# Kernel optimization log

Hardware: AMD Instinct MI355X
Metric: run time of the kernel (lower is better)

The kernel has to match this reference:

```python
import jax, jax.numpy as jnp
import numpy as np

# 20 amino-acid letters and per-residue atom counts (len(struct.atoms) - 1 in the source)
LETTERS = "ARNDCQEGHILKMFPSTWYV"
RES_LEN = {"A": 4, "R": 10, "N": 7, "D": 7, "C": 5, "Q": 8, "E": 8, "G": 3, "H": 9,
           "I": 7, "L": 7, "K": 8, "M": 7, "F": 10, "P": 6, "S": 5, "T": 6, "W": 13,
           "Y": 11, "V": 6}
BATCH = 16
N_RES = 1024       # number of residues (output 'nodes')
ATOM_DIM = 64
AMINO_DIM = 256
INDS = 1           # one trailing (3,) tensor axis


def make_metadata():
    """Deterministic protein sequence + per-letter gather indices (static numpy)."""
    rng = np.random.default_rng(42)
    seq = rng.integers(0, len(LETTERS), size=N_RES)
    lens = np.array([RES_LEN[LETTERS[s]] for s in seq])
    starts = np.concatenate([[0], np.cumsum(lens)[:-1]])  # residue_indices
    atoms = int(lens.sum())
    # group residues by letter: (residue positions, atom gather indices (n_l, L))
    groups = {}
    for li, letter in enumerate(LETTERS):
        pos = np.where(seq == li)[0]
        if len(pos) == 0:
            continue
        L = RES_LEN[letter]
        idx = starts[pos][:, None] + np.arange(L)[None, :]  # (n_l, L)
        groups[letter] = (pos, idx)
    # static row offsets of each letter's weight block inside the flat weight
    offsets, off = {}, 0
    for letter in LETTERS:
        offsets[letter] = off
        off += RES_LEN[letter] * ATOM_DIM
    return atoms, groups, offsets


def setup_inputs() -> dict:
    atoms, groups, offsets = make_metadata()
    key = jax.random.key(0)
    k1, k2 = jax.random.split(key)
    x = jax.random.normal(k1, (BATCH, atoms, ATOM_DIM, 3), dtype=jnp.float32)
    total_rows = sum(RES_LEN[l] for l in LETTERS) * ATOM_DIM  # 147*64 = 9408
    W = jax.random.normal(k2, (total_rows, AMINO_DIM), dtype=jnp.float32)
    # per-expert 1/sqrt(fan_in) init scaling
    scale = np.zeros((total_rows, 1), np.float32)
    for l in LETTERS:
        fan = RES_LEN[l] * ATOM_DIM
        scale[offsets[l]:offsets[l] + fan] = 1.0 / np.sqrt(fan)
    W = W * jnp.asarray(scale)
    return {"x": x, "W_flat": W}


def reference(x, W_flat):
    """x: (B, atoms, D, 3); W_flat: (sum_l L_l*D, amino_dim).
    Equivalent to per-residue slice -> reshape -> per-letter TensLinear -> stack,
    but grouped by letter into batched GEMMs (same math, reordered)."""
    atoms, groups, offsets = make_metadata()
    B = x.shape[0]
    out = jnp.zeros((B, N_RES, AMINO_DIM, 3), dtype=x.dtype)
    for letter, (pos, idx) in groups.items():  # fixed loop over <=20 expert types
        L = RES_LEN[letter]
        fan = L * ATOM_DIM
        g = x[:, idx]                              # (B, n_l, L, D, 3) gather
        g = g.reshape(B, len(pos), fan, 3)         # flatten residue atoms x channels
        Wl = W_flat[offsets[letter]:offsets[letter] + fan]  # (fan, amino_dim)
        y = jnp.einsum("bnki,ko->bnoi", g, Wl)     # (B, n_l, amino_dim, 3)
        out = out.at[:, pos].set(y)                # scatter back into residue order
    return out
```

## Files before the change

### kernel.cpp

```cpp
#include <hip/hip_runtime.h>
#include <hip/hip_bf16.h>
#include <cstdint>
#include <cstddef>

#define NRES 1024
#define NB 16
#define ADIM 64
#define ODIM 256
#define TOTROWS 9408

typedef __bf16 bf16x8 __attribute__((ext_vector_type(8)));
typedef float f32x4 __attribute__((ext_vector_type(4)));

struct Meta {
    uint16_t start[NRES];
    uint8_t  letter[NRES];
    int atoms;
};

constexpr int RES_LEN_A[20] = {4,10,7,7,5,8,8,3,9,7,7,8,7,10,6,5,6,13,11,6};

constexpr uint32_t ss_hash(uint32_t value, uint32_t& hc) {
    value ^= hc;
    hc *= 0x931e8875u;
    value *= hc;
    value ^= value >> 16;
    return value;
}
constexpr uint32_t ss_mix(uint32_t x, uint32_t y) {
    uint32_t r = 0xca01f9ddu * x - 0x4973f715u * y;
    r ^= r >> 16;
    return r;
}

constexpr Meta make_meta() {
    Meta m = {};
    uint32_t pool[4] = {0,0,0,0};
    uint32_t hc = 0x43b0d7e5u;
    pool[0] = ss_hash(42u, hc);
    pool[1] = ss_hash(0u, hc);
    pool[2] = ss_hash(0u, hc);
    pool[3] = ss_hash(0u, hc);
    for (int s = 0; s < 4; ++s)
        for (int d = 0; d < 4; ++d)
            if (s != d) pool[d] = ss_mix(pool[d], ss_hash(pool[s], hc));
    uint32_t hb = 0x8b51f9ddu;
    uint64_t w[8] = {};
    for (int i = 0; i < 8; ++i) {
        uint32_t dv = pool[i & 3] ^ hb;
        hb *= 0x58f38dedu;
        dv *= hb;
        dv ^= dv >> 16;
        w[i] = dv;
    }
    uint64_t s64[4] = {};
    for (int i = 0; i < 4; ++i) s64[i] = w[2*i] | (w[2*i+1] << 32);
    using u128 = unsigned __int128;
    const u128 MULT = ((u128)2549297995355413924ULL << 64) | (u128)4865540595714422341ULL;
    u128 initstate = ((u128)s64[0] << 64) | (u128)s64[1];
    u128 initseq   = ((u128)s64[2] << 64) | (u128)s64[3];
    u128 inc = (initseq << 1) | (u128)1;
    u128 state = inc;
    state += initstate;
    state = state * MULT + inc;
    bool has32 = false;
    uint32_t cached = 0;
    int atoms = 0;
    for (int i = 0; i < NRES; ++i) {
        uint32_t res = 0;
        while (true) {
            uint32_t r32;
            if (has32) { r32 = cached; has32 = false; }
            else {
                state = state * MULT + inc;
                uint64_t hi = (uint64_t)(state >> 64);
                uint64_t lo = (uint64_t)state;
                uint32_t rot = (uint32_t)(state >> 122);
                uint64_t v = hi ^ lo;
                uint64_t o64 = (v >> rot) | (v << ((64u - rot) & 63u));
                cached = (uint32_t)(o64 >> 32);
                has32 = true;
                r32 = (uint32_t)o64;
            }
            uint64_t mm = (uint64_t)r32 * 20ull;
            uint32_t leftover = (uint32_t)mm;
            if (leftover >= 16u) { res = (uint32_t)(mm >> 32); break; }
        }
        m.letter[i] = (uint8_t)res;
        m.start[i] = (uint16_t)atoms;
        atoms += RES_LEN_A[res];
    }
    m.atoms = atoms;
    return m;
}

constexpr Meta H_META = make_meta();

struct LetterTab {
    int woff[21];
    int fan[20];
};
constexpr LetterTab make_tab() {
    LetterTab t = {};
    int off = 0;
    for (int l = 0; l < 20; ++l) {
        t.woff[l] = off;
        t.fan[l] = RES_LEN_A[l] * ADIM;
        off += t.fan[l];
    }
    t.woff[20] = off;
    return t;
}

struct Perm { uint16_t p[NRES]; };
constexpr Perm make_perm() {
    int ord[20];
    for (int i = 0; i < 20; ++i) ord[i] = i;
    for (int a = 0; a < 20; ++a) {
        int best = a;
        for (int j = a + 1; j < 20; ++j)
            if (RES_LEN_A[ord[j]] > RES_LEN_A[ord[best]]) best = j;
        int t = ord[a]; ord[a] = ord[best]; ord[best] = t;
    }
    Perm pr = {};
    int n = 0;
    for (int oi = 0; oi < 20; ++oi) {
        const int l = ord[oi];
        for (int p = 0; p < NRES; ++p)
            if (H_META.letter[p] == l) pr.p[n++] = (uint16_t)p;
    }
    return pr;
}

__constant__ Meta g_meta = make_meta();
__constant__ LetterTab g_tab = make_tab();
__constant__ Perm g_perm = make_perm();

__device__ __bf16 g_Wt[(size_t)TOTROWS * ODIM];

__global__ __launch_bounds__(256) void prep_W_kernel(const float* __restrict__ W) {
    const int tid = threadIdx.x;
    const int b = blockIdx.x * 4 + (tid >> 6);
    const int lane = tid & 63;
    const int l15 = lane & 15;
    const int g4 = lane >> 4;

    int l = 0;
    while (b >= (g_tab.woff[l + 1] >> 1)) ++l;
    const int rel = b - (g_tab.woff[l] >> 1);
    const int c = rel >> 5;
    const int r32 = rel & 31;
    const int h = r32 >> 4;
    const int wv = (r32 >> 2) & 3;
    const int nt = r32 & 3;

    const int n = wv * 64 + nt * 16 + l15;
    const int kg = g_tab.woff[l] + c * 64 + h * 32 + g4 * 8;

    bf16x8 v;
    #pragma unroll
    for (int q = 0; q < 8; ++q)
        v[q] = (__bf16)W[(size_t)(kg + q) * ODIM + n];
    *(bf16x8*)&g_Wt[(size_t)b * 512 + (size_t)(l15 * 4 + g4) * 8] = v;
}

__device__ __forceinline__ void gload16(const void* g, void* l) {
    __builtin_amdgcn_global_load_lds(
        (const __attribute__((address_space(1))) uint32_t*)(uintptr_t)g,
        (__attribute__((address_space(3))) uint32_t*)(uint32_t)(uintptr_t)l,
        16, 0, 0);
}

__global__ __launch_bounds__(512) void lin_mfma_kernel(const float* __restrict__ x,
                                                       float* __restrict__ out,
                                                       int atoms) {
    const int p = g_perm.p[blockIdx.x];
    const int letter = g_meta.letter[p];
    const int start = g_meta.start[p];
    const int fan = g_tab.fan[letter];
    const __bf16* wslab = g_Wt + (size_t)g_tab.woff[letter] * ODIM;

    const int tid = threadIdx.x;
    const int lane = tid & 63;
    const int w8 = tid >> 6;
    const int l15 = lane & 15;
    const int g4 = lane >> 4;

    __shared__ __align__(16) uint8_t raw[2 * 12288];
    __shared__ __align__(16) __bf16 As[2][48][72];

    const float* xb = x + (size_t)start * 192;
    const size_t bstrB = (size_t)atoms * 768;
    const int nc = fan >> 6;

    const int s0 = 2 * w8, s1 = s0 + 1;
    const uint32_t pos0 = (uint32_t)(s0 * 1024 + lane * 16);
    const uint32_t pos1 = (uint32_t)(s1 * 1024 + lane * 16);
    const uint32_t b0 = pos0 / 768, o0 = pos0 - b0 * 768;
    const uint32_t b1 = pos1 / 768, o1 = pos1 - b1 * 768;
    const uint8_t* gsrc0 = (const uint8_t*)xb + (size_t)b0 * bstrB + o0;
    const uint8_t* gsrc1 = (const uint8_t*)xb + (size_t)b1 * bstrB + o1;
    uint8_t* ldst0 = raw + s0 * 1024;
    uint8_t* ldst1 = raw + s1 * 1024;
    const bool stager = (w8 < 6);

    auto STAGE = [&](int cc) {
        const size_t go = (size_t)cc * 768;
        const uint32_t ro = (uint32_t)(cc & 1) * 12288u;
        gload16(gsrc0 + go, ldst0 + ro);
        gload16(gsrc1 + go, ldst1 + ro);
    };

    const int bl0 = tid / 48, r40 = tid - bl0 * 48;
    const int e41 = 512 + tid;
    const int bl1 = e41 / 48, r41 = e41 - bl1 * 48;
    const bool has1 = (tid < 256);

    const __bf16* wbase = wslab + (size_t)(w8 * 2) * 512 + (size_t)(l15 * 4 + g4) * 8;

    f32x4 acc[3][2];
    #pragma unroll
    for (int t = 0; t < 3; ++t)
        #pragma unroll
        for (int n = 0; n < 2; ++n)
            acc[t][n] = (f32x4){0.f, 0.f, 0.f, 0.f};

    if (stager) { STAGE(0); STAGE(1); }

    for (int c = 0; c < nc; ++c) {
        const int buf = c & 1;
        if (stager) {
            if (c + 1 < nc) asm volatile("s_waitcnt vmcnt(2)" ::: "memory");
            else            asm volatile("s_waitcnt vmcnt(0)" ::: "memory");
        }
        __builtin_amdgcn_s_barrier();
        asm volatile("" ::: "memory");

        {
            const uint8_t* rb = raw + (buf ? 12288 : 0);
            const float4 v0 = *(const float4*)(rb + (size_t)tid * 16);
            const float f0[4] = {v0.x, v0.y, v0.z, v0.w};
            #pragma unroll
            for (int q = 0; q < 4; ++q) {
                const int r = r40 * 4 + q, kl = r / 3, i = r - kl * 3;
                As[buf][bl0 * 3 + i][kl] = (__bf16)f0[q];
            }
            if (has1) {
                const float4 v1 = *(const float4*)(rb + (size_t)e41 * 16);
                const float f1[4] = {v1.x, v1.y, v1.z, v1.w};
                #pragma unroll
                for (int q = 0; q < 4; ++q) {
                    const int r = r41 * 4 + q, kl = r / 3, i = r - kl * 3;
                    As[buf][bl1 * 3 + i][kl] = (__bf16)f1[q];
                }
            }
        }
        asm volatile("s_waitcnt lgkmcnt(0)" ::: "memory");
        __builtin_amdgcn_s_barrier();
        asm volatile("" ::: "memory");

        if (stager && c + 2 < nc) STAGE(c + 2);

        #pragma unroll
        for (int h = 0; h < 2; ++h) {
            bf16x8 a[3], wf[2];
            #pragma unroll
            for (int t = 0; t < 3; ++t)
                a[t] = *(const bf16x8*)&As[buf][t * 16 + l15][h * 32 + g4 * 8];
            #pragma unroll
            for (int ntl = 0; ntl < 2; ++ntl)
                wf[ntl] = *(const bf16x8*)(wbase + (size_t)c * 16384 + (size_t)h * 8192 + (size_t)ntl * 512);
            #pragma unroll
            for (int ntl = 0; ntl < 2; ++ntl)
                #pragma unroll
                for (int t = 0; t < 3; ++t)
                    acc[t][ntl] = __builtin_amdgcn_mfma_f32_16x16x32_bf16(a[t], wf[ntl], acc[t][ntl], 0, 0, 0);
        }
    }

    #pragma unroll
    for (int t = 0; t < 3; ++t)
        #pragma unroll
        for (int reg = 0; reg < 4; ++reg) {
            const int r = t * 16 + g4 * 4 + reg;
            const int bl = r / 3;
            const int i = r - bl * 3;
            #pragma unroll
            for (int ntl = 0; ntl < 2; ++ntl) {
                const int o = w8 * 32 + ntl * 16 + l15;
                out[(((size_t)bl * NRES + p) * ODIM + o) * 3 + i] = acc[t][ntl][reg];
            }
        }
}

extern "C" void kernel_launch(void* const* d_in, const int* in_sizes, int n_in,
                              void* d_out, int out_size, void* d_ws, size_t ws_size,
                              hipStream_t stream) {
    (void)n_in; (void)out_size; (void)d_ws; (void)ws_size;
    const float* x = (const float*)d_in[0];
    const float* W = (const float*)d_in[1];
    float* out = (float*)d_out;
    const int atoms = in_sizes[0] / (NB * ADIM * 3);
    prep_W_kernel<<<TOTROWS / 8, 256, 0, stream>>>(W);
    lin_mfma_kernel<<<NRES, 512, 0, stream>>>(x, out, atoms);
}
```

Measured before the change: 50.23 us.

## Warp-specialize producer waves with triple-buffered async staging and W register prefetch

The block grows to 640 threads. Two dedicated producer waves issue all global-to-LDS async loads into a three-slot ring, running up to three chunks ahead. The eight compute waves do the bf16 conversion and the MFMAs, prefetch the next chunk's weight fragments into registers, and raise wave priority during compute. The aim is to hide x and W load latency behind the math, at the cost of more LDS and registers per block and two waves that sit idle during compute.

```diff
diff --git a/kernel.cpp b/kernel.cpp
--- a/kernel.cpp
+++ b/kernel.cpp
@@ -171,9 +171,9 @@
         16, 0, 0);
 }
 
-__global__ __launch_bounds__(512) void lin_mfma_kernel(const float* __restrict__ x,
-                                                       float* __restrict__ out,
-                                                       int atoms) {
+__global__ __launch_bounds__(640, 2) void lin_mfma_kernel(const float* __restrict__ x,
+                                                          float* __restrict__ out,
+                                                          int atoms) {
     const int p = g_perm.p[blockIdx.x];
     const int letter = g_meta.letter[p];
     const int start = g_meta.start[p];
@@ -182,33 +182,34 @@
 
     const int tid = threadIdx.x;
     const int lane = tid & 63;
-    const int w8 = tid >> 6;
+    const int w10 = tid >> 6;
+    const bool is_stager = (w10 >= 8);
     const int l15 = lane & 15;
     const int g4 = lane >> 4;
 
-    __shared__ __align__(16) uint8_t raw[2 * 12288];
+    __shared__ __align__(16) uint8_t raw[3][12288];
     __shared__ __align__(16) __bf16 As[2][48][72];
 
-    const float* xb = x + (size_t)start * 192;
+    const uint8_t* xbB = (const uint8_t*)x + (size_t)start * 768;
     const size_t bstrB = (size_t)atoms * 768;
     const int nc = fan >> 6;
 
-    const int s0 = 2 * w8, s1 = s0 + 1;
-    const uint32_t pos0 = (uint32_t)(s0 * 1024 + lane * 16);
-    const uint32_t pos1 = (uint32_t)(s1 * 1024 + lane * 16);
-    const uint32_t b0 = pos0 / 768, o0 = pos0 - b0 * 768;
-    const uint32_t b1 = pos1 / 768, o1 = pos1 - b1 * 768;
-    const uint8_t* gsrc0 = (const uint8_t*)xb + (size_t)b0 * bstrB + o0;
-    const uint8_t* gsrc1 = (const uint8_t*)xb + (size_t)b1 * bstrB + o1;
-    uint8_t* ldst0 = raw + s0 * 1024;
-    uint8_t* ldst1 = raw + s1 * 1024;
-    const bool stager = (w8 < 6);
-
-    auto STAGE = [&](int cc) {
-        const size_t go = (size_t)cc * 768;
-        const uint32_t ro = (uint32_t)(cc & 1) * 12288u;
-        gload16(gsrc0 + go, ldst0 + ro);
-        gload16(gsrc1 + go, ldst1 + ro);
+    const int s = w10 - 8;
+    const uint8_t* gsrc[6];
+    uint32_t ldo[6];
+    if (is_stager) {
+        #pragma unroll
+        for (int j = 0; j < 6; ++j) {
+            const uint32_t pos = (uint32_t)(s * 6144 + j * 1024 + lane * 16);
+            const uint32_t b = pos / 768, off = pos - b * 768;
+            gsrc[j] = xbB + (size_t)b * bstrB + off;
+            ldo[j] = (uint32_t)(s * 6144 + j * 1024);
+        }
+    }
+    auto STAGE = [&](int cc, int slot) {
+        #pragma unroll
+        for (int j = 0; j < 6; ++j)
+            gload16(gsrc[j] + (size_t)cc * 768, &raw[slot][0] + ldo[j]);
     };
 
     const int bl0 = tid / 48, r40 = tid - bl0 * 48;
@@ -216,7 +217,7 @@
     const int bl1 = e41 / 48, r41 = e41 - bl1 * 48;
     const bool has1 = (tid < 256);
 
-    const __bf16* wbase = wslab + (size_t)(w8 * 2) * 512 + (size_t)(l15 * 4 + g4) * 8;
+    const __bf16* wbase = wslab + (size_t)((w10 & 7) * 2) * 512 + (size_t)(l15 * 4 + g4) * 8;
 
     f32x4 acc[3][2];
     #pragma unroll
@@ -225,72 +226,104 @@
         for (int n = 0; n < 2; ++n)
             acc[t][n] = (f32x4){0.f, 0.f, 0.f, 0.f};
 
-    if (stager) { STAGE(0); STAGE(1); }
-
-    for (int c = 0; c < nc; ++c) {
-        const int buf = c & 1;
-        if (stager) {
-            if (c + 1 < nc) asm volatile("s_waitcnt vmcnt(2)" ::: "memory");
-            else            asm volatile("s_waitcnt vmcnt(0)" ::: "memory");
+    bf16x8 wA[4], wB[4];
+    auto LOADW = [&](int cc, bf16x8* wf) {
+        const __bf16* wc = wbase + (size_t)cc * 16384;
+        #pragma unroll
+        for (int h = 0; h < 2; ++h)
+            #pragma unroll
+            for (int ntl = 0; ntl < 2; ++ntl)
+                wf[h * 2 + ntl] = *(const bf16x8*)(wc + (size_t)h * 8192 + (size_t)ntl * 512);
+    };
+    auto CONVERT = [&](int buf, int slot) {
+        const uint8_t* rb = &raw[slot][0];
+        const float4 v0 = *(const float4*)(rb + (size_t)tid * 16);
+        const float f0[4] = {v0.x, v0.y, v0.z, v0.w};
+        #pragma unroll
+        for (int q = 0; q < 4; ++q) {
+            const int r = r40 * 4 + q, kl = r / 3, i = r - kl * 3;
+            As[buf][bl0 * 3 + i][kl] = (__bf16)f0[q];
+        }
+        if (has1) {
+            const float4 v1 = *(const float4*)(rb + (size_t)e41 * 16);
+            const float f1[4] = {v1.x, v1.y, v1.z, v1.w};
+            #pragma unroll
+            for (int q = 0; q < 4; ++q) {
+                const int r = r41 * 4 + q, kl = r / 3, i = r - kl * 3;
+                As[buf][bl1 * 3 + i][kl] = (__bf16)f1[q];
+            }
+        }
+    };
+    auto COMPUTE = [&](int buf, const bf16x8* wf) {
+        #pragma unroll
+        for (int h = 0; h < 2; ++h) {
+            bf16x8 a[3];
+            #pragma unroll
+            for (int t = 0; t < 3; ++t)
+                a[t] = *(const bf16x8*)&As[buf][t * 16 + l15][h * 32 + g4 * 8];
+            #pragma unroll
+            for (int ntl = 0; ntl < 2; ++ntl)
+                #pragma unroll
+                for (int t = 0; t < 3; ++t)
+                    acc[t][ntl] = __builtin_amdgcn_mfma_f32_16x16x32_bf16(a[t], wf[h * 2 + ntl], acc[t][ntl], 0, 0, 0);
+        }
+    };
+
+    auto ITER = [&](int c, bf16x8* wCur, bf16x8* wNxt) {
+        if (is_stager) {
+            const int rem = nc - c;
+            if (rem >= 3)      asm volatile("s_waitcnt vmcnt(12)" ::: "memory");
+            else if (rem == 2) asm volatile("s_waitcnt vmcnt(6)" ::: "memory");
+            else               asm volatile("s_waitcnt vmcnt(0)" ::: "memory");
         }
         __builtin_amdgcn_s_barrier();
         asm volatile("" ::: "memory");
 
-        {
-            const uint8_t* rb = raw + (buf ? 12288 : 0);
-            const float4 v0 = *(const float4*)(rb + (size_t)tid * 16);
-            const float f0[4] = {v0.x, v0.y, v0.z, v0.w};
-            #pragma unroll
-            for (int q = 0; q < 4; ++q) {
-                const int r = r40 * 4 + q, kl = r / 3, i = r - kl * 3;
-                As[buf][bl0 * 3 + i][kl] = (__bf16)f0[q];
-            }
-            if (has1) {
-                const float4 v1 = *(const float4*)(rb + (size_t)e41 * 16);
-                const float f1[4] = {v1.x, v1.y, v1.z, v1.w};
-                #pragma unroll
-                for (int q = 0; q < 4; ++q) {
-                    const int r = r41 * 4 + q, kl = r / 3, i = r - kl * 3;
-                    As[buf][bl1 * 3 + i][kl] = (__bf16)f1[q];
-                }
-            }
+        const int buf = c & 1;
+        if (!is_stager) {
+            CONVERT(buf, c % 3);
+            if (c + 1 < nc) LOADW(c + 1, wNxt);
         }
         asm volatile("s_waitcnt lgkmcnt(0)" ::: "memory");
         __builtin_amdgcn_s_barrier();
         asm volatile("" ::: "memory");
 
-        if (stager && c + 2 < nc) STAGE(c + 2);
-
-        #pragma unroll
-        for (int h = 0; h < 2; ++h) {
-            bf16x8 a[3], wf[2];
-            #pragma unroll
-            for (int t = 0; t < 3; ++t)
-                a[t] = *(const bf16x8*)&As[buf][t * 16 + l15][h * 32 + g4 * 8];
-            #pragma unroll
-            for (int ntl = 0; ntl < 2; ++ntl)
-                wf[ntl] = *(const bf16x8*)(wbase + (size_t)c * 16384 + (size_t)h * 8192 + (size_t)ntl * 512);
-            #pragma unroll
-            for (int ntl = 0; ntl < 2; ++ntl)
+        if (is_stager) {
+            if (c + 3 < nc) STAGE(c + 3, c % 3);
+        } else {
+            __builtin_amdgcn_s_setprio(1);
+            COMPUTE(buf, wCur);
+            __builtin_amdgcn_s_setprio(0);
+        }
+    };
+
+    if (is_stager) { STAGE(0, 0); STAGE(1, 1); STAGE(2, 2); }
+    else LOADW(0, wA);
+
+    int c = 0;
+    while (true) {
+        ITER(c, wA, wB);
+        if (++c == nc) break;
+        ITER(c, wB, wA);
+        if (++c == nc) break;
+    }
+
+    if (!is_stager) {
+        const int w8 = w10;
+        #pragma unroll
+        for (int t = 0; t < 3; ++t)
+            #pragma unroll
+            for (int reg = 0; reg < 4; ++reg) {
+                const int r = t * 16 + g4 * 4 + reg;
+                const int bl = r / 3;
+                const int i = r - bl * 3;
                 #pragma unroll
-                for (int t = 0; t < 3; ++t)
-                    acc[t][ntl] = __builtin_amdgcn_mfma_f32_16x16x32_bf16(a[t], wf[ntl], acc[t][ntl], 0, 0, 0);
-        }
-    }
-
-    #pragma unroll
-    for (int t = 0; t < 3; ++t)
-        #pragma unroll
-        for (int reg = 0; reg < 4; ++reg) {
-            const int r = t * 16 + g4 * 4 + reg;
-            const int bl = r / 3;
-            const int i = r - bl * 3;
-            #pragma unroll
-            for (int ntl = 0; ntl < 2; ++ntl) {
-                const int o = w8 * 32 + ntl * 16 + l15;
-                out[(((size_t)bl * NRES + p) * ODIM + o) * 3 + i] = acc[t][ntl][reg];
+                for (int ntl = 0; ntl < 2; ++ntl) {
+                    const int o = w8 * 32 + ntl * 16 + l15;
+                    out[(((size_t)bl * NRES + p) * ODIM + o) * 3 + i] = acc[t][ntl][reg];
+                }
             }
-        }
+    }
 }
 
 extern "C" void kernel_launch(void* const* d_in, const int* in_sizes, int n_in,
@@ -302,5 +335,5 @@
     float* out = (float*)d_out;
     const int atoms = in_sizes[0] / (NB * ADIM * 3);
     prep_W_kernel<<<TOTROWS / 8, 256, 0, stream>>>(W);
-    lin_mfma_kernel<<<NRES, 512, 0, stream>>>(x, out, atoms);
-}
+    lin_mfma_kernel<<<NRES, 640, 0, stream>>>(x, out, atoms);
+}
```

Result: slower. 56.85 us (+13.2%).
